# Optimization experiments

Measured on AMD Instinct MI355X. Metric: run time of the kernel, lower is better.

## Reference

```python
import jax, jax.numpy as jnp
import numpy as np

# B batch, N seq (n_vec), V vocab, D model dim, H heads, DH head dim,
# L depth, WS window size, R landmark rank, C classes
B, N, V, D, H, DH, L, WS, R, C = 4, 4096, 512, 512, 8, 64, 4, 128, 256, 10
FF = 4 * D
SCALE = DH ** -0.5


def _ln(t, g, b, eps=1e-5):
    mu = jnp.mean(t, axis=-1, keepdims=True)
    var = jnp.var(t, axis=-1, keepdims=True)
    return (t - mu) * jax.lax.rsqrt(var + eps) * g + b


def setup_inputs():
    key = jax.random.key(0)
    ks = iter(jax.random.split(key, 16))

    def w(shape, s=0.02):
        return (jax.random.normal(next(ks), shape) * s).astype(jnp.float32)

    return dict(
        x=jax.random.randint(next(ks), (B, N), 0, V, dtype=jnp.int32),
        tok_emb=w((V, D)), pos_emb=w((N, D)),
        ln1_g=jnp.ones((L, D), jnp.float32), ln1_b=jnp.zeros((L, D), jnp.float32),
        Wq=w((L, D, H * DH)), Wkv=w((L, D, 2 * H * DH)), Wp=w((L, DH, R)),
        lln_g=jnp.ones((L, DH), jnp.float32), lln_b=jnp.zeros((L, DH), jnp.float32),
        gln_g=jnp.ones((L, DH), jnp.float32), gln_b=jnp.zeros((L, DH), jnp.float32),
        Wo=w((L, H * DH, D)), bo=jnp.zeros((L, D), jnp.float32),
        ln2_g=jnp.ones((L, D), jnp.float32), ln2_b=jnp.zeros((L, D), jnp.float32),
        W1=w((L, D, FF)), b1=jnp.zeros((L, FF), jnp.float32),
        W2=w((L, FF, D)), b2=jnp.zeros((L, D), jnp.float32),
        lnf_g=jnp.ones((D,), jnp.float32), lnf_b=jnp.zeros((D,), jnp.float32),
        Wlog=w((D, V)), blog=jnp.zeros((V,), jnp.float32),
        Wfin=w((N * V, C), 0.005), bfin=jnp.zeros((C,), jnp.float32),
    )


def _forward(x, tok_emb, pos_emb, ln1_g, ln1_b, Wq, Wkv, Wp, lln_g, lln_b,
             gln_g, gln_b, Wo, bo, ln2_g, ln2_b, W1, b1, W2, b2,
             lnf_g, lnf_b, Wlog, blog, Wfin, bfin):
    h = tok_emb[x] + pos_emb[None, :, :]  # [B,N,D]
    nw = N // WS
    for l in range(L):
        # ---- PreNorm Long-Short attention ----
        y = _ln(h, ln1_g[l], ln1_b[l])
        q = (y @ Wq[l]).reshape(B, N, H, DH).transpose(0, 2, 1, 3) * SCALE  # [B,H,N,DH]
        kv = (y @ Wkv[l]).reshape(B, N, 2, H, DH).transpose(2, 0, 3, 1, 4)
        k, v = kv[0], kv[1]  # [B,H,N,DH]
        # dynamic low-rank landmark projection: softmax over the sequence dim
        p = jax.nn.softmax(jnp.einsum('bhnd,dr->bhnr', k, Wp[l]), axis=2)
        gk = _ln(jnp.einsum('bhnr,bhnd->bhrd', p, k), gln_g[l], gln_b[l])  # [B,H,R,DH]
        gv = _ln(jnp.einsum('bhnr,bhnd->bhrd', p, v), gln_g[l], gln_b[l])
        # DualLN on the short-range (local window) keys/values
        lk = _ln(k, lln_g[l], lln_b[l]).reshape(B, H, nw, WS, DH)
        lv = _ln(v, lln_g[l], lln_b[l]).reshape(B, H, nw, WS, DH)
        lq = q.reshape(B, H, nw, WS, DH)
        sim_l = jnp.einsum('bhnwd,bhnxd->bhnwx', lq, lk)  # [B,H,nw,WS,WS]
        sim_g = jnp.einsum('bhnwd,bhrd->bhnwr', lq, gk)   # [B,H,nw,WS,R]
        attn = jax.nn.softmax(jnp.concatenate([sim_l, sim_g], axis=-1), axis=-1)
        a_l, a_g = attn[..., :WS], attn[..., WS:]
        o = (jnp.einsum('bhnwx,bhnxd->bhnwd', a_l, lv)
             + jnp.einsum('bhnwr,bhrd->bhnwd', a_g, gv))
        o = o.reshape(B, H, N, DH).transpose(0, 2, 1, 3).reshape(B, N, H * DH)
        h = h + o @ Wo[l] + bo[l]
        # ---- PreNorm FeedForward ----
        y = _ln(h, ln2_g[l], ln2_b[l])
        h = h + jax.nn.gelu(y @ W1[l] + b1[l]) @ W2[l] + b2[l]
    logits = _ln(h, lnf_g, lnf_b) @ Wlog + blog  # [B,N,V]
    # FLATTEN pooling head (dropout is identity in eval mode)
    return logits.reshape(B, N * V) @ Wfin + bfin  # [B,C]


def reference(x, tok_emb, pos_emb, ln1_g, ln1_b, Wq, Wkv, Wp, lln_g, lln_b,
              gln_g, gln_b, Wo, bo, ln2_g, ln2_b, W1, b1, W2, b2,
              lnf_g, lnf_b, Wlog, blog, Wfin, bfin):
    return _forward(x, tok_emb, pos_emb, ln1_g, ln1_b, Wq, Wkv, Wp, lln_g, lln_b,
                    gln_g, gln_b, Wo, bo, ln2_g, ln2_b, W1, b1, W2, b2,
                    lnf_g, lnf_b, Wlog, blog, Wfin, bfin)
```

## Files before the change

### kernel.cpp

```cpp
#include <hip/hip_runtime.h>
#include <hip/hip_bf16.h>

typedef unsigned short u16;
typedef __attribute__((ext_vector_type(8))) short short8;
typedef __attribute__((ext_vector_type(4))) float floatx4;

#define FLAG_GELU   1
#define FLAG_ACC    2
#define FLAG_NN     4
#define FLAG_CF32   8
#define FLAG_ATOMIC 16

__device__ __forceinline__ float bf2f(u16 u){
  union { unsigned u; float f; } c; c.u = ((unsigned)u)<<16; return c.f;
}
__device__ __forceinline__ u16 f2bf(float f){
  union { float f; unsigned u; } c; c.f = f;
  unsigned r = (c.u + 0x7fffu + ((c.u>>16)&1u))>>16;
  return (u16)r;
}
__device__ __forceinline__ float rdin(const void* base, long long idx, int flagv){
  return flagv ? ((const float*)base)[idx] : bf2f(((const u16*)base)[idx]);
}
__device__ __forceinline__ float fast_gelu(float x){
  float u = 0.7978845608028654f*(x + 0.044715f*x*x*x);
  float e = __expf(2.f*u);
  float t = 1.f - 2.f/(e+1.f);
  return 0.5f*x*(1.f+t);
}

__global__ void detect_kernel(const void* tok, int* flag){
  __shared__ int cnt;
  if(threadIdx.x==0) cnt=0;
  __syncthreads();
  float v = fabsf(bf2f(((const u16*)tok)[threadIdx.x]));
  int bad = (v < 1e3f) ? 0 : 1;
  atomicAdd(&cnt, bad);
  __syncthreads();
  if(threadIdx.x==0) *flag = (cnt>0) ? 1 : 0;
}

__global__ void cvtT_kernel(const void* src, long long off0, long long zstride, u16* __restrict__ dst,
    long long dzstride, int K, int N, const int* flag){
  __shared__ float tl[32][33];
  int fl = *flag;
  int k0 = blockIdx.x*32, n0 = blockIdx.y*32;
  long long base = off0 + (long long)blockIdx.z*zstride;
  for(int i=threadIdx.y;i<32;i+=8){
    long long idx = base + (long long)(k0+i)*N + n0 + threadIdx.x;
    tl[i][threadIdx.x] = fl ? ((const float*)src)[idx] : bf2f(((const u16*)src)[idx]);
  }
  __syncthreads();
  u16* dz = dst + (long long)blockIdx.z*dzstride;
  for(int i=threadIdx.y;i<32;i+=8)
    dz[(long long)(n0+i)*K + k0 + threadIdx.x] = f2bf(tl[threadIdx.x][i]);
}

__global__ void transposeB_kernel(const u16* __restrict__ in, u16* __restrict__ out,
    long long izs0, long long izs1, int zd, long long ozstride, int ldin, int ldout){
  __shared__ u16 tl[32][33];
  int z = blockIdx.z; int z0 = z/zd, z1 = z - z0*zd;
  const u16* ip = in + z0*izs0 + z1*izs1;
  u16* op = out + (long long)z*ozstride;
  int r0 = blockIdx.x*32, c0 = blockIdx.y*32;
  for(int i=threadIdx.y;i<32;i+=8)
    tl[i][threadIdx.x] = ip[(long long)(r0+i)*ldin + c0 + threadIdx.x];
  __syncthreads();
  for(int i=threadIdx.y;i<32;i+=8)
    op[(long long)(c0+i)*ldout + r0 + threadIdx.x] = tl[threadIdx.x][i];
}

__global__ __launch_bounds__(256) void zerof_kernel(float* p, int n){
  int i = blockIdx.x*256 + threadIdx.x;
  if(i<n) p[i]=0.f;
}

struct GemmP {
  const u16* A; const u16* B; float* Cf; u16* Ch;
  const void* bias; int biasOff; const int* dflag;
  int K, lda, ldb, ldc;
  long long sA0,sA1,sA2,sB0,sB1,sB2,sC0,sC1,sC2;
  int d0,d1; float alpha; int flags; int ksplit;
};

__global__ __launch_bounds__(256) void gemm_kernel(GemmP p){
  __shared__ __align__(16) u16 As[64][40];
  __shared__ __align__(16) u16 Bs[64][40];
  int z = blockIdx.z;
  int i0 = z / p.d0; int rem = z - i0*p.d0; int i1 = rem / p.d1; int i2 = rem - i1*p.d1;
  const u16* A  = p.A + i0*p.sA0 + i1*p.sA1 + i2*p.sA2;
  const u16* Bp = p.B + i0*p.sB0 + i1*p.sB1 + i2*p.sB2;
  long long cb = i0*p.sC0 + i1*p.sC1 + i2*p.sC2;
  int kbeg = 0, kend = p.K;
  if(p.ksplit){ kbeg = i1*p.ksplit; kend = kbeg + p.ksplit; }
  int m0 = blockIdx.x*64, n0 = blockIdx.y*64;
  int t = threadIdx.x, lane = t&63, wave = t>>6;
  int wm = (wave>>1)*32, wn = (wave&1)*32;
  int quad = lane>>4, l16 = lane&15;
  floatx4 zero4 = {0.f,0.f,0.f,0.f};
  floatx4 acc00=zero4, acc01=zero4, acc10=zero4, acc11=zero4;
  int sr = t>>2, sc = (t&3)*8;
  int bkr = t>>3, bnc = (t&7)*8;
  bool nn = (p.flags & FLAG_NN);
  for(int k0=kbeg;k0<kend;k0+=32){
    uint4 av = *(const uint4*)(A + (long long)(m0+sr)*p.lda + (k0+sc));
    uint4 bv;
    if(nn) bv = *(const uint4*)(Bp + (long long)(k0+bkr)*p.ldb + (n0+bnc));
    else   bv = *(const uint4*)(Bp + (long long)(n0+sr)*p.ldb + (k0+sc));
    *(uint4*)&As[sr][sc] = av;
    if(nn){
      u16 tmp[8]; *(uint4*)tmp = bv;
      #pragma unroll
      for(int j=0;j<8;j++) Bs[bnc+j][bkr] = tmp[j];
    } else {
      *(uint4*)&Bs[sr][sc] = bv;
    }
    __syncthreads();
    short8 a0 = *(const short8*)&As[wm+l16][quad*8];
    short8 a1 = *(const short8*)&As[wm+16+l16][quad*8];
    short8 b0 = *(const short8*)&Bs[wn+l16][quad*8];
    short8 b1 = *(const short8*)&Bs[wn+16+l16][quad*8];
    acc00 = __builtin_amdgcn_mfma_f32_16x16x32_bf16(a0,b0,acc00,0,0,0);
    acc01 = __builtin_amdgcn_mfma_f32_16x16x32_bf16(a0,b1,acc01,0,0,0);
    acc10 = __builtin_amdgcn_mfma_f32_16x16x32_bf16(a1,b0,acc10,0,0,0);
    acc11 = __builtin_amdgcn_mfma_f32_16x16x32_bf16(a1,b1,acc11,0,0,0);
    __syncthreads();
  }
  int flagv = p.bias ? *p.dflag : 0;
  #pragma unroll
  for(int mi=0;mi<2;mi++){
    #pragma unroll
    for(int ni=0;ni<2;ni++){
      floatx4 a = (mi==0)?((ni==0)?acc00:acc01):((ni==0)?acc10:acc11);
      int cg = n0 + wn + ni*16 + l16;
      float bv_ = p.bias ? rdin(p.bias, (long long)p.biasOff + cg, flagv) : 0.f;
      #pragma unroll
      for(int e=0;e<4;e++){
        int rg = m0 + wm + mi*16 + quad*4 + e;
        float v = a[e]*p.alpha + bv_;
        if(p.flags & FLAG_GELU) v = fast_gelu(v);
        long long ci = cb + (long long)rg*p.ldc + cg;
        if(p.flags & FLAG_ATOMIC){
          atomicAdd(&p.Cf[ci], v);
        } else if(p.flags & FLAG_CF32){
          float o2 = v; if(p.flags&FLAG_ACC) o2 += p.Cf[ci];
          p.Cf[ci] = o2;
        } else {
          float o2 = v; if(p.flags&FLAG_ACC) o2 += bf2f(p.Ch[ci]);
          p.Ch[ci] = f2bf(o2);
        }
      }
    }
  }
}

struct Gemm128P {
  const u16* A; const u16* B; float* Cf; u16* Ch;
  const void* bias; int biasOff; const int* dflag;
  int K, lda, ldb, ldc; float alpha; int flags;
};

template<int BM>
__global__ __launch_bounds__(512) void gemm2ph_kernel(Gemm128P p){
  constexpr int NA   = BM/64;
  constexpr int HH   = BM/2;
  constexpr int MI   = HH/16;
  constexpr int ABUF = BM*64;
  constexpr int LDSZ = (BM==256) ? 69632 : 49152;
  __shared__ __align__(16) u16 lds[LDSZ];
  u16* As = lds;
  u16* Bs = lds + 2*ABUF;
  int m0 = blockIdx.x*BM, n0 = blockIdx.y*256;
  int t = threadIdx.x, lane = t&63, wave = t>>6;
  int quad = lane>>4, l16 = lane&15;
  int wr = wave>>2, wc = wave&3;
  int rowA = t>>3, colk = (t&7)*8;
  const u16* Asrc[NA];
  const u16* Bsrc[4];
  #pragma unroll
  for(int q=0;q<NA;q++) Asrc[q] = p.A + (long long)(m0 + q*64 + rowA)*p.lda + colk;
  #pragma unroll
  for(int q=0;q<4;q++)  Bsrc[q] = p.B + (long long)(n0 + q*64 + rowA)*p.ldb + colk;
  int nk = p.K >> 6;
  floatx4 acc[MI][4] = {};

  auto stage = [&](int buf, int k0){
    #pragma unroll
    for(int q=0;q<NA;q++)
      __builtin_amdgcn_global_load_lds(
        (const __attribute__((address_space(1))) unsigned int*)(Asrc[q] + k0),
        (__attribute__((address_space(3))) unsigned int*)(As + buf*ABUF + q*4096 + wave*512),
        16, 0, 0);
    #pragma unroll
    for(int q=0;q<4;q++)
      __builtin_amdgcn_global_load_lds(
        (const __attribute__((address_space(1))) unsigned int*)(Bsrc[q] + k0),
        (__attribute__((address_space(3))) unsigned int*)(Bs + buf*16384 + q*4096 + wave*512),
        16, 0, 0);
  };

  stage(0, 0);
  __syncthreads();
  for(int kt=0; kt<nk; ++kt){
    int cur = kt&1;
    if(kt+1 < nk) stage(cur^1, (kt+1)*64);
    const u16* Ab = As + cur*ABUF;
    const u16* Bb = Bs + cur*16384;
    #pragma unroll
    for(int ks=0; ks<2; ks++){
      short8 a[MI], b[4];
      #pragma unroll
      for(int i=0;i<MI;i++)
        a[i] = *(const short8*)&Ab[(wr*HH + i*16 + l16)*64 + ks*32 + quad*8];
      #pragma unroll
      for(int j=0;j<4;j++)
        b[j] = *(const short8*)&Bb[(wc*64 + j*16 + l16)*64 + ks*32 + quad*8];
      #pragma unroll
      for(int i=0;i<MI;i++)
        #pragma unroll
        for(int j=0;j<4;j++)
          acc[i][j] = __builtin_amdgcn_mfma_f32_16x16x32_bf16(a[i], b[j], acc[i][j],0,0,0);
    }
    __syncthreads();
  }

  int flagv = p.bias ? *p.dflag : 0;
  if(!(p.flags & FLAG_CF32)){
    u16* Ct = lds + wave*(HH*68);
    #pragma unroll
    for(int j=0;j<4;j++){
      int cg = n0 + wc*64 + j*16 + l16;
      float bv_ = p.bias ? rdin(p.bias, (long long)p.biasOff + cg, flagv) : 0.f;
      #pragma unroll
      for(int i=0;i<MI;i++){
        #pragma unroll
        for(int e=0;e<4;e++){
          float v = acc[i][j][e]*p.alpha + bv_;
          if(p.flags & FLAG_GELU) v = fast_gelu(v);
          Ct[(i*16 + quad*4 + e)*68 + j*16 + l16] = f2bf(v);
        }
      }
    }
    int rsub = lane>>3, csub = (lane&7)*8;
    #pragma unroll
    for(int rr=0; rr<HH/8; rr++){
      int row = rr*8 + rsub;
      uint4 v = *(const uint4*)&Ct[row*68 + csub];
      *(uint4*)(p.Ch + (long long)(m0 + wr*HH + row)*p.ldc + (n0 + wc*64 + csub)) = v;
    }
  } else {
    #pragma unroll
    for(int j=0;j<4;j++){
      int cg = n0 + wc*64 + j*16 + l16;
      float bv_ = p.bias ? rdin(p.bias, (long long)p.biasOff + cg, flagv) : 0.f;
      #pragma unroll
      for(int i=0;i<MI;i++){
        #pragma unroll
        for(int e=0;e<4;e++){
          int rg = m0 + wr*HH + i*16 + quad*4 + e;
          float v = acc[i][j][e]*p.alpha + bv_;
          if(p.flags & FLAG_GELU) v = fast_gelu(v);
          long long ci = (long long)rg*p.ldc + cg;
          float o2 = v; if(p.flags&FLAG_ACC) o2 += p.Cf[ci];
          p.Cf[ci] = o2;
        }
      }
    }
  }
}

struct AttnP {
  const u16* q;
  const u16* k;
  const u16* gk;
  const u16* vT;
  const u16* gvT;
  u16* o;
};

__global__ __launch_bounds__(256) void attn_kernel(AttnP p){
  __shared__ __align__(16) u16 S[4][12544];
  __shared__ float ssum[4][32];
  const int SST = 392;
  int w = blockIdx.x, bh = blockIdx.y;
  int b = bh>>3, hh = bh&7;
  int t = threadIdx.x, lane = t&63, wave = t>>6;
  int quad = lane>>4, l16 = lane&15;
  u16* Sw = &S[wave][0];
  int mbase = w*128 + wave*32;
  short8 aq[2][2];
  #pragma unroll
  for(int mt=0;mt<2;mt++)
    #pragma unroll
    for(int kc=0;kc<2;kc++)
      aq[mt][kc] = *(const short8*)(p.q + ((long long)b*4096 + mbase + mt*16 + l16)*512 + hh*64 + kc*32 + quad*8);
  for(int ct=0; ct<24; ct++){
    short8 bf0, bf1;
    if(ct<8){
      const u16* kr = p.k + ((long long)b*4096 + w*128 + ct*16 + l16)*1024 + hh*64;
      bf0 = *(const short8*)(kr + quad*8);
      bf1 = *(const short8*)(kr + 32 + quad*8);
    } else {
      const u16* gr = p.gk + ((long long)bh*256 + (ct-8)*16 + l16)*64;
      bf0 = *(const short8*)(gr + quad*8);
      bf1 = *(const short8*)(gr + 32 + quad*8);
    }
    #pragma unroll
    for(int mt=0;mt<2;mt++){
      floatx4 acc = {0.f,0.f,0.f,0.f};
      acc = __builtin_amdgcn_mfma_f32_16x16x32_bf16(aq[mt][0], bf0, acc,0,0,0);
      acc = __builtin_amdgcn_mfma_f32_16x16x32_bf16(aq[mt][1], bf1, acc,0,0,0);
      #pragma unroll
      for(int e=0;e<4;e++)
        Sw[(mt*16 + quad*4 + e)*SST + ct*16 + l16] = f2bf(acc[e]);
    }
  }
  __syncthreads();
  {
    int r = lane&31, ph = lane>>5;
    u16* Srow = Sw + r*SST + ph*192;
    float mmax = -3.4e38f;
    u16 buf[8];
    for(int it=0; it<24; it++){
      *(uint4*)buf = *(const uint4*)(Srow + it*8);
      #pragma unroll
      for(int j=0;j<8;j++) mmax = fmaxf(mmax, bf2f(buf[j]));
    }
    mmax = fmaxf(mmax, __shfl_xor(mmax, 32));
    float s = 0.f;
    for(int it=0; it<24; it++){
      *(uint4*)buf = *(const uint4*)(Srow + it*8);
      #pragma unroll
      for(int j=0;j<8;j++){ float e_ = __expf(bf2f(buf[j]) - mmax); s += e_; buf[j] = f2bf(e_); }
      *(uint4*)(Srow + it*8) = *(uint4*)buf;
    }
    s += __shfl_xor(s, 32);
    if(ph==0) ssum[wave][r] = 1.f/s;
  }
  __syncthreads();
  floatx4 oacc[2][4] = {};
  for(int kc=0; kc<12; kc++){
    short8 ap0 = *(const short8*)(Sw + (l16)*SST + kc*32 + quad*8);
    short8 ap1 = *(const short8*)(Sw + (16 + l16)*SST + kc*32 + quad*8);
    #pragma unroll
    for(int dt=0; dt<4; dt++){
      short8 bv;
      if(kc<4)
        bv = *(const short8*)(p.vT + (long long)bh*262144 + (dt*16+l16)*4096 + w*128 + kc*32 + quad*8);
      else
        bv = *(const short8*)(p.gvT + (long long)bh*16384 + (dt*16+l16)*256 + (kc-4)*32 + quad*8);
      oacc[0][dt] = __builtin_amdgcn_mfma_f32_16x16x32_bf16(ap0, bv, oacc[0][dt],0,0,0);
      oacc[1][dt] = __builtin_amdgcn_mfma_f32_16x16x32_bf16(ap1, bv, oacc[1][dt],0,0,0);
    }
  }
  #pragma unroll
  for(int mt=0;mt<2;mt++){
    #pragma unroll
    for(int e=0;e<4;e++){
      int row = mt*16 + quad*4 + e;
      float inv = ssum[wave][row];
      long long obase = ((long long)b*4096 + mbase + row)*512 + hh*64;
      #pragma unroll
      for(int dt=0;dt<4;dt++)
        p.o[obase + dt*16 + l16] = f2bf(oacc[mt][dt][e]*inv);
    }
  }
}

__global__ __launch_bounds__(256) void embed_kernel(const int* __restrict__ x, const void* tok,
    const void* pos, float* __restrict__ h, const int* flag){
  int i = blockIdx.x*256 + threadIdx.x;
  int flagv = *flag;
  int d = i & 511;
  int n = (i>>9) & 4095;
  int bn = i>>9;
  int tid2 = x[bn];
  h[i] = rdin(tok, (long long)tid2*512 + d, flagv) + rdin(pos, (long long)n*512 + d, flagv);
}

__global__ __launch_bounds__(256) void ln512_kernel(const float* __restrict__ h,
    const void* g, const void* b, int goff, u16* __restrict__ y, const int* flag){
  int row = blockIdx.x;
  int flagv = *flag;
  const float* hr = h + (size_t)row*512;
  int t = threadIdx.x;
  float x0 = hr[t], x1 = hr[t+256];
  float s1 = x0+x1, s2 = x0*x0+x1*x1;
  for(int o=32;o>0;o>>=1){ s1 += __shfl_down(s1,o,64); s2 += __shfl_down(s2,o,64); }
  __shared__ float sh1[4], sh2[4];
  int wv=t>>6, ln=t&63;
  if(ln==0){ sh1[wv]=s1; sh2[wv]=s2; }
  __syncthreads();
  float st = sh1[0]+sh1[1]+sh1[2]+sh1[3];
  float qt = sh2[0]+sh2[1]+sh2[2]+sh2[3];
  float mu = st*(1.f/512.f);
  float var = qt*(1.f/512.f) - mu*mu;
  float inv = rsqrtf(var+1e-5f);
  u16* yr = y + (size_t)row*512;
  yr[t]     = f2bf((x0-mu)*inv*rdin(g,goff+t,flagv)     + rdin(b,goff+t,flagv));
  yr[t+256] = f2bf((x1-mu)*inv*rdin(g,goff+t+256,flagv) + rdin(b,goff+t+256,flagv));
}

__global__ __launch_bounds__(256) void ln64_kernel(const u16* __restrict__ in, const float* __restrict__ inF,
    u16* __restrict__ out, const void* g, const void* b, int goff,
    long long s0, long long s1v, long long s2v, int d0, int d1, const int* flag){
  int r = blockIdx.x*4 + (threadIdx.x>>6);
  int ln = threadIdx.x&63;
  int flagv = *flag;
  int i0 = r/d0; int rem = r - i0*d0; int i1 = rem/d1; int i2 = rem - i1*d1;
  long long off = i0*s0 + i1*s1v + i2*s2v;
  float x = inF ? inF[off+ln] : bf2f(in[off + ln]);
  float s = x, sq = x*x;
  for(int o=32;o>0;o>>=1){ s += __shfl_down(s,o,64); sq += __shfl_down(sq,o,64); }
  s = __shfl(s,0,64); sq = __shfl(sq,0,64);
  float mu = s*(1.f/64.f), var = sq*(1.f/64.f)-mu*mu;
  float inv = rsqrtf(var+1e-5f);
  out[off + ln] = f2bf((x-mu)*inv*rdin(g,goff+ln,flagv) + rdin(b,goff+ln,flagv));
}

__global__ __launch_bounds__(256) void softmax4096_kernel(u16* __restrict__ p){
  u16* pr = p + (size_t)blockIdx.x*4096;
  int t = threadIdx.x;
  u16 tmp[16];
  *(uint4*)tmp     = *(const uint4*)(pr + t*16);
  *(uint4*)(tmp+8) = *(const uint4*)(pr + t*16 + 8);
  float xs[16]; float m=-3.4e38f;
  #pragma unroll
  for(int i=0;i<16;i++){ xs[i]=bf2f(tmp[i]); m=fmaxf(m,xs[i]); }
  for(int o=32;o>0;o>>=1) m = fmaxf(m, __shfl_down(m,o,64));
  __shared__ float sm[4]; __shared__ float sv[4];
  int wv=t>>6, ln=t&63;
  if(ln==0) sm[wv]=m;
  __syncthreads();
  m = fmaxf(fmaxf(sm[0],sm[1]),fmaxf(sm[2],sm[3]));
  float s=0;
  #pragma unroll
  for(int i=0;i<16;i++){ xs[i]=__expf(xs[i]-m); s+=xs[i]; }
  for(int o=32;o>0;o>>=1) s += __shfl_down(s,o,64);
  if(ln==0) sv[wv]=s;
  __syncthreads();
  s = sv[0]+sv[1]+sv[2]+sv[3];
  float inv = 1.f/s;
  #pragma unroll
  for(int i=0;i<16;i++) tmp[i]=f2bf(xs[i]*inv);
  *(uint4*)(pr + t*16)     = *(uint4*)tmp;
  *(uint4*)(pr + t*16 + 8) = *(uint4*)(tmp+8);
}

__global__ void zero40_kernel(float* p){ if(threadIdx.x<40) p[threadIdx.x]=0.f; }

__global__ __launch_bounds__(256) void head_kernel(const float* __restrict__ logits,
    const void* wfin, float* __restrict__ part, const int* flag){
  int b = blockIdx.x>>7, chunk = blockIdx.x&127;
  int flagv = *flag;
  const float* lr = logits + (size_t)b*2097152 + (size_t)chunk*16384;
  float acc[10];
  #pragma unroll
  for(int c=0;c<10;c++) acc[c]=0.f;
  for(int j=threadIdx.x;j<16384;j+=256){
    float lv_ = lr[j];
    long long wb = (long long)(chunk*16384 + j)*10;
    if(flagv){
      const float* w = (const float*)wfin + wb;
      #pragma unroll
      for(int c=0;c<10;c++) acc[c] += lv_*w[c];
    } else {
      const u16* w = (const u16*)wfin + wb;
      #pragma unroll
      for(int c=0;c<10;c++) acc[c] += lv_*bf2f(w[c]);
    }
  }
  __shared__ float red[4];
  int wv=threadIdx.x>>6, ln=threadIdx.x&63;
  for(int c=0;c<10;c++){
    float v=acc[c];
    for(int o=32;o>0;o>>=1) v+=__shfl_down(v,o,64);
    __syncthreads();
    if(ln==0) red[wv]=v;
    __syncthreads();
    if(threadIdx.x==0) atomicAdd(&part[b*10+c], red[0]+red[1]+red[2]+red[3]);
  }
}

__global__ void fin_kernel(const float* __restrict__ part, const void* bfin, void* out, const int* flag){
  int i=threadIdx.x;
  int flagv = *flag;
  if(i<40){
    float r = part[i] + rdin(bfin, i%10, flagv);
    if(flagv) ((float*)out)[i] = r;
    else      ((u16*)out)[i]   = f2bf(r);
  }
}

static const size_t OFF_H    = 0;
static const size_t OFF_Y    = 33554432;
static const size_t OFF_GKF  = 33554432;
static const size_t OFF_GVF  = 35651584;
static const size_t OFF_Q    = 50331648;
static const size_t OFF_KV   = 67108864;
static const size_t OFF_GK   = 100663296;
static const size_t OFF_GV   = 101711872;
static const size_t OFF_BIG  = 102760448;
static const size_t OFF_KT   = 169869312;
static const size_t OFF_VT   = 186646528;
static const size_t OFF_WTP  = 203423744;
static const size_t OFF_WQT  = 203554816;
static const size_t OFF_WKVT = 204079104;
static const size_t OFF_WOT  = 205127680;
static const size_t OFF_W1T  = 205651968;
static const size_t OFF_W2T  = 207749120;
static const size_t OFF_PART = 209846272;
static const size_t OFF_FLAG = 209846528;
static const size_t WS_NEED  = 209846784;

static inline GemmP mkg(const void*A,const void*B,void*C,const void*bias,int biasOff,const int* dflag,
  int K,int lda,int ldb,int ldc,
  long long a0,long long a1,long long a2,long long b0,long long b1,long long b2,
  long long c0,long long c1,long long c2,int d0,int d1,float alpha,int flags,int ksplit){
  GemmP p; p.A=(const u16*)A; p.B=(const u16*)B;
  p.Cf=(float*)C; p.Ch=(u16*)C; p.bias=bias; p.biasOff=biasOff; p.dflag=dflag;
  p.K=K;p.lda=lda;p.ldb=ldb;p.ldc=ldc;
  p.sA0=a0;p.sA1=a1;p.sA2=a2;p.sB0=b0;p.sB1=b1;p.sB2=b2;p.sC0=c0;p.sC1=c1;p.sC2=c2;
  p.d0=d0;p.d1=d1;p.alpha=alpha;p.flags=flags;p.ksplit=ksplit; return p;
}
static inline Gemm128P mk128(const void*A,const void*B,void*C,const void*bias,int biasOff,const int* dflag,
  int K,int lda,int ldb,int ldc,float alpha,int flags){
  Gemm128P p; p.A=(const u16*)A; p.B=(const u16*)B;
  p.Cf=(float*)C; p.Ch=(u16*)C; p.bias=bias; p.biasOff=biasOff; p.dflag=dflag;
  p.K=K;p.lda=lda;p.ldb=ldb;p.ldc=ldc;p.alpha=alpha;p.flags=flags; return p;
}

extern "C" void kernel_launch(void* const* d_in, const int* in_sizes, int n_in,
                              void* d_out, int out_size, void* d_ws, size_t ws_size,
                              hipStream_t stream){
  (void)in_sizes;(void)n_in;(void)out_size;
  if(ws_size < WS_NEED) return;
  const int*  x    = (const int*)d_in[0];
  const void* tok  = d_in[1];
  const void* pos  = d_in[2];
  const void* ln1g = d_in[3];
  const void* ln1b = d_in[4];
  const void* Wq   = d_in[5];
  const void* Wkv  = d_in[6];
  const void* Wp   = d_in[7];
  const void* llng = d_in[8];
  const void* llnb = d_in[9];
  const void* glng = d_in[10];
  const void* glnb = d_in[11];
  const void* Wo   = d_in[12];
  const void* bo   = d_in[13];
  const void* ln2g = d_in[14];
  const void* ln2b = d_in[15];
  const void* W1   = d_in[16];
  const void* b1   = d_in[17];
  const void* W2   = d_in[18];
  const void* b2   = d_in[19];
  const void* lnfg = d_in[20];
  const void* lnfb = d_in[21];
  const void* Wlog = d_in[22];
  const void* blog = d_in[23];
  const void* Wfin = d_in[24];
  const void* bfin = d_in[25];

  char* ws = (char*)d_ws;
  float* h    = (float*)(ws + OFF_H);
  u16* y      = (u16*)(ws + OFF_Y);
  u16* ob     = (u16*)(ws + OFF_Y);
  float* gkF  = (float*)(ws + OFF_GKF);
  float* gvF  = (float*)(ws + OFF_GVF);
  u16* qb     = (u16*)(ws + OFF_Q);
  u16* kv     = (u16*)(ws + OFF_KV);
  u16* gk     = (u16*)(ws + OFF_GK);
  u16* gv     = (u16*)(ws + OFF_GV);
  u16* big    = (u16*)(ws + OFF_BIG);
  float* bigf = (float*)(ws + OFF_BIG);
  u16* kT     = (u16*)(ws + OFF_KT);
  u16* gvT    = (u16*)(ws + OFF_KT);
  u16* vT     = (u16*)(ws + OFF_VT);
  u16* wTp    = (u16*)(ws + OFF_WTP);
  u16* sWqT   = (u16*)(ws + OFF_WQT);
  u16* sWkvT  = (u16*)(ws + OFF_WKVT);
  u16* sWoT   = (u16*)(ws + OFF_WOT);
  u16* sW1T   = (u16*)(ws + OFF_W1T);
  u16* sW2T   = (u16*)(ws + OFF_W2T);
  float* part = (float*)(ws + OFF_PART);
  int* flag   = (int*)(ws + OFF_FLAG);

  dim3 tb(32,8);
  detect_kernel<<<dim3(1),dim3(256),0,stream>>>(tok, flag);
  cvtT_kernel<<<dim3(2,8,4),tb,0,stream>>>(Wp, 0, 16384, wTp, 16384, 64, 256, flag);
  embed_kernel<<<dim3(32768),dim3(256),0,stream>>>(x, tok, pos, h, flag);

  for(int l=0;l<4;l++){
    cvtT_kernel<<<dim3(16,16,1),tb,0,stream>>>(Wq,  (long long)l*262144,  0, sWqT,  0, 512, 512,  flag);
    cvtT_kernel<<<dim3(16,32,1),tb,0,stream>>>(Wkv, (long long)l*524288,  0, sWkvT, 0, 512, 1024, flag);
    cvtT_kernel<<<dim3(16,16,1),tb,0,stream>>>(Wo,  (long long)l*262144,  0, sWoT,  0, 512, 512,  flag);
    cvtT_kernel<<<dim3(16,64,1),tb,0,stream>>>(W1,  (long long)l*1048576, 0, sW1T,  0, 512, 2048, flag);
    cvtT_kernel<<<dim3(64,16,1),tb,0,stream>>>(W2,  (long long)l*1048576, 0, sW2T,  0, 2048, 512, flag);

    ln512_kernel<<<dim3(16384),dim3(256),0,stream>>>(h, ln1g, ln1b, l*512, y, flag);
    { Gemm128P p = mk128(y, sWqT, qb, nullptr,0,flag, 512,512,512,512, 0.125f, 0);
      gemm2ph_kernel<128><<<dim3(128,2),512,0,stream>>>(p); }
    { Gemm128P p = mk128(y, sWkvT, kv, nullptr,0,flag, 512,512,512,1024, 1.f, 0);
      gemm2ph_kernel<256><<<dim3(64,4),512,0,stream>>>(p); }
    zerof_kernel<<<dim3(4096),dim3(256),0,stream>>>(gkF, 1048576);
    { GemmP p = mkg(wTp + (size_t)l*16384, kv, big, nullptr,0,flag, 64,64,1024,4096,
        0,0,0, 4194304LL,64,0, 8388608LL,1048576LL,0, 8,1, 1.f, 0, 0);
      gemm_kernel<<<dim3(4,64,32),256,0,stream>>>(p); }
    softmax4096_kernel<<<dim3(8192),dim3(256),0,stream>>>(big);
    transposeB_kernel<<<dim3(128,2,32),tb,0,stream>>>(kv,     kT, 4194304LL,64,8, 262144LL, 1024, 4096);
    transposeB_kernel<<<dim3(128,2,32),tb,0,stream>>>(kv+512, vT, 4194304LL,64,8, 262144LL, 1024, 4096);
    { GemmP p = mkg(big, kT, gkF, nullptr,0,flag, 4096,4096,4096,64,
        1048576LL,0,0, 262144LL,0,0, 16384LL,0,0, 8,1, 1.f, FLAG_CF32|FLAG_ATOMIC, 512);
      gemm_kernel<<<dim3(4,1,256),256,0,stream>>>(p); }
    { GemmP p = mkg(big, vT, gvF, nullptr,0,flag, 4096,4096,4096,64,
        1048576LL,0,0, 262144LL,0,0, 16384LL,0,0, 8,1, 1.f, FLAG_CF32|FLAG_ATOMIC, 512);
      gemm_kernel<<<dim3(4,1,256),256,0,stream>>>(p); }
    ln64_kernel<<<dim3(2048),dim3(256),0,stream>>>(gk, gkF, gk, glng, glnb, l*64, 64,1,1, 1,1, flag);
    ln64_kernel<<<dim3(2048),dim3(256),0,stream>>>(gv, gvF, gv, glng, glnb, l*64, 64,1,1, 1,1, flag);
    ln64_kernel<<<dim3(32768),dim3(256),0,stream>>>(kv,     nullptr, kv,     llng, llnb, l*64, 4194304LL,64,1024, 32768,4096, flag);
    ln64_kernel<<<dim3(32768),dim3(256),0,stream>>>(kv+512, nullptr, kv+512, llng, llnb, l*64, 4194304LL,64,1024, 32768,4096, flag);
    transposeB_kernel<<<dim3(128,2,32),tb,0,stream>>>(kv+512, vT, 4194304LL,64,8, 262144LL, 1024, 4096);
    transposeB_kernel<<<dim3(8,2,32),tb,0,stream>>>(gv, gvT, 16384LL,0,1, 16384LL, 64, 256);
    { AttnP ap; ap.q=qb; ap.k=kv; ap.gk=gk; ap.vT=vT; ap.gvT=gvT; ap.o=ob;
      attn_kernel<<<dim3(32,32),256,0,stream>>>(ap); }
    { Gemm128P p = mk128(ob, sWoT, h, bo,l*512,flag, 512,512,512,512, 1.f, FLAG_ACC|FLAG_CF32);
      gemm2ph_kernel<128><<<dim3(128,2),512,0,stream>>>(p); }
    ln512_kernel<<<dim3(16384),dim3(256),0,stream>>>(h, ln2g, ln2b, l*512, y, flag);
    { Gemm128P p = mk128(y, sW1T, big, b1,l*2048,flag, 512,512,512,2048, 1.f, FLAG_GELU);
      gemm2ph_kernel<256><<<dim3(64,8),512,0,stream>>>(p); }
    { Gemm128P p = mk128(big, sW2T, h, b2,l*512,flag, 2048,2048,2048,512, 1.f, FLAG_ACC|FLAG_CF32);
      gemm2ph_kernel<128><<<dim3(128,2),512,0,stream>>>(p); }
  }
  ln512_kernel<<<dim3(16384),dim3(256),0,stream>>>(h, lnfg, lnfb, 0, y, flag);
  cvtT_kernel<<<dim3(16,16,1),tb,0,stream>>>(Wlog, 0, 0, sWqT, 0, 512, 512, flag);
  { Gemm128P p = mk128(y, sWqT, bigf, blog,0,flag, 512,512,512,512, 1.f, FLAG_CF32);
    gemm2ph_kernel<128><<<dim3(128,2),512,0,stream>>>(p); }
  zero40_kernel<<<dim3(1),dim3(64),0,stream>>>(part);
  head_kernel<<<dim3(512),dim3(256),0,stream>>>(bigf, Wfin, part, flag);
  fin_kernel<<<dim3(1),dim3(64),0,stream>>>(part, bfin, d_out, flag);
}
```

Before: 2.559 ms.

## Split attention work across waves per 32-row query block

The attention kernel now assigns one 32-row query block per workgroup, with four times as many blocks. Its four waves split the score columns (6 tiles each), the softmax rows (8 threads per row with shuffle reductions) and the output head-dim tiles (one per wave). This cuts LDS use per block and register pressure per wave, aiming for higher occupancy and more parallelism. In exchange, each block reloads the same Q rows into every wave, and each block now re-reads the K/V window and global keys/values for fewer query rows, so global and L2 traffic goes up.

After: 2.476 ms. 3.3% less time.

```diff
diff --git a/kernel.cpp b/kernel.cpp
--- a/kernel.cpp
+++ b/kernel.cpp
@@ -279,22 +279,25 @@
 };
 
 __global__ __launch_bounds__(256) void attn_kernel(AttnP p){
-  __shared__ __align__(16) u16 S[4][12544];
-  __shared__ float ssum[4][32];
+  __shared__ __align__(16) u16 S[32*392];
+  __shared__ float ssum[32];
   const int SST = 392;
-  int w = blockIdx.x, bh = blockIdx.y;
+  int qb = blockIdx.x;
+  int bh = blockIdx.y;
   int b = bh>>3, hh = bh&7;
+  int w = qb>>2;
   int t = threadIdx.x, lane = t&63, wave = t>>6;
   int quad = lane>>4, l16 = lane&15;
-  u16* Sw = &S[wave][0];
-  int mbase = w*128 + wave*32;
+  int mbase = qb*32;
   short8 aq[2][2];
   #pragma unroll
   for(int mt=0;mt<2;mt++)
     #pragma unroll
     for(int kc=0;kc<2;kc++)
       aq[mt][kc] = *(const short8*)(p.q + ((long long)b*4096 + mbase + mt*16 + l16)*512 + hh*64 + kc*32 + quad*8);
-  for(int ct=0; ct<24; ct++){
+  #pragma unroll
+  for(int i=0;i<6;i++){
+    int ct = wave*6 + i;
     short8 bf0, bf1;
     if(ct<8){
       const u16* kr = p.k + ((long long)b*4096 + w*128 + ct*16 + l16)*1024 + hh*64;
@@ -312,57 +315,55 @@
       acc = __builtin_amdgcn_mfma_f32_16x16x32_bf16(aq[mt][1], bf1, acc,0,0,0);
       #pragma unroll
       for(int e=0;e<4;e++)
-        Sw[(mt*16 + quad*4 + e)*SST + ct*16 + l16] = f2bf(acc[e]);
+        S[(mt*16 + quad*4 + e)*SST + ct*16 + l16] = f2bf(acc[e]);
     }
   }
   __syncthreads();
   {
-    int r = lane&31, ph = lane>>5;
-    u16* Srow = Sw + r*SST + ph*192;
+    int r = t>>3, seg = t&7;
+    u16* Srow = S + r*SST + seg*48;
+    u16 buf[48];
+    #pragma unroll
+    for(int it=0; it<6; it++)
+      *(uint4*)(buf + it*8) = *(const uint4*)(Srow + it*8);
     float mmax = -3.4e38f;
-    u16 buf[8];
-    for(int it=0; it<24; it++){
-      *(uint4*)buf = *(const uint4*)(Srow + it*8);
-      #pragma unroll
-      for(int j=0;j<8;j++) mmax = fmaxf(mmax, bf2f(buf[j]));
-    }
-    mmax = fmaxf(mmax, __shfl_xor(mmax, 32));
+    #pragma unroll
+    for(int j=0;j<48;j++) mmax = fmaxf(mmax, bf2f(buf[j]));
+    mmax = fmaxf(mmax, __shfl_xor(mmax, 1));
+    mmax = fmaxf(mmax, __shfl_xor(mmax, 2));
+    mmax = fmaxf(mmax, __shfl_xor(mmax, 4));
     float s = 0.f;
-    for(int it=0; it<24; it++){
-      *(uint4*)buf = *(const uint4*)(Srow + it*8);
-      #pragma unroll
-      for(int j=0;j<8;j++){ float e_ = __expf(bf2f(buf[j]) - mmax); s += e_; buf[j] = f2bf(e_); }
-      *(uint4*)(Srow + it*8) = *(uint4*)buf;
-    }
-    s += __shfl_xor(s, 32);
-    if(ph==0) ssum[wave][r] = 1.f/s;
-  }
-  __syncthreads();
-  floatx4 oacc[2][4] = {};
+    #pragma unroll
+    for(int j=0;j<48;j++){ float e_ = __expf(bf2f(buf[j]) - mmax); s += e_; buf[j] = f2bf(e_); }
+    #pragma unroll
+    for(int it=0; it<6; it++)
+      *(uint4*)(Srow + it*8) = *(const uint4*)(buf + it*8);
+    s += __shfl_xor(s, 1);
+    s += __shfl_xor(s, 2);
+    s += __shfl_xor(s, 4);
+    if(seg==0) ssum[r] = 1.f/s;
+  }
+  __syncthreads();
+  int dt = wave;
+  floatx4 oacc[2] = {};
   for(int kc=0; kc<12; kc++){
-    short8 ap0 = *(const short8*)(Sw + (l16)*SST + kc*32 + quad*8);
-    short8 ap1 = *(const short8*)(Sw + (16 + l16)*SST + kc*32 + quad*8);
-    #pragma unroll
-    for(int dt=0; dt<4; dt++){
-      short8 bv;
-      if(kc<4)
-        bv = *(const short8*)(p.vT + (long long)bh*262144 + (dt*16+l16)*4096 + w*128 + kc*32 + quad*8);
-      else
-        bv = *(const short8*)(p.gvT + (long long)bh*16384 + (dt*16+l16)*256 + (kc-4)*32 + quad*8);
-      oacc[0][dt] = __builtin_amdgcn_mfma_f32_16x16x32_bf16(ap0, bv, oacc[0][dt],0,0,0);
-      oacc[1][dt] = __builtin_amdgcn_mfma_f32_16x16x32_bf16(ap1, bv, oacc[1][dt],0,0,0);
-    }
+    short8 ap0 = *(const short8*)(S + (l16)*SST + kc*32 + quad*8);
+    short8 ap1 = *(const short8*)(S + (16 + l16)*SST + kc*32 + quad*8);
+    short8 bv;
+    if(kc<4)
+      bv = *(const short8*)(p.vT + (long long)bh*262144 + (dt*16+l16)*4096 + w*128 + kc*32 + quad*8);
+    else
+      bv = *(const short8*)(p.gvT + (long long)bh*16384 + (dt*16+l16)*256 + (kc-4)*32 + quad*8);
+    oacc[0] = __builtin_amdgcn_mfma_f32_16x16x32_bf16(ap0, bv, oacc[0],0,0,0);
+    oacc[1] = __builtin_amdgcn_mfma_f32_16x16x32_bf16(ap1, bv, oacc[1],0,0,0);
   }
   #pragma unroll
   for(int mt=0;mt<2;mt++){
     #pragma unroll
     for(int e=0;e<4;e++){
       int row = mt*16 + quad*4 + e;
-      float inv = ssum[wave][row];
-      long long obase = ((long long)b*4096 + mbase + row)*512 + hh*64;
-      #pragma unroll
-      for(int dt=0;dt<4;dt++)
-        p.o[obase + dt*16 + l16] = f2bf(oacc[mt][dt][e]*inv);
+      float inv = ssum[row];
+      p.o[((long long)b*4096 + mbase + row)*512 + hh*64 + dt*16 + l16] = f2bf(oacc[mt][e]*inv);
     }
   }
 }
@@ -623,7 +624,7 @@
     transposeB_kernel<<<dim3(128,2,32),tb,0,stream>>>(kv+512, vT, 4194304LL,64,8, 262144LL, 1024, 4096);
     transposeB_kernel<<<dim3(8,2,32),tb,0,stream>>>(gv, gvT, 16384LL,0,1, 16384LL, 64, 256);
     { AttnP ap; ap.q=qb; ap.k=kv; ap.gk=gk; ap.vT=vT; ap.gvT=gvT; ap.o=ob;
-      attn_kernel<<<dim3(32,32),256,0,stream>>>(ap); }
+      attn_kernel<<<dim3(128,32),256,0,stream>>>(ap); }
     { Gemm128P p = mk128(ob, sWoT, h, bo,l*512,flag, 512,512,512,512, 1.f, FLAG_ACC|FLAG_CF32);
       gemm2ph_kernel<128><<<dim3(128,2),512,0,stream>>>(p); }
     ln512_kernel<<<dim3(16384),dim3(256),0,stream>>>(h, ln2g, ln2b, l*512, y, flag);
```
